# Kernel optimization log

Measured on AMD Instinct MI355X. Metric: run time of the kernel, lower is better.

The kernel has to match this reference:

```python
import jax, jax.numpy as jnp
import numpy as np
from jax.scipy.special import logsumexp

NTRANS = 40          # 2 * nbase * (nbase + 1) with nbase = 4
NBASE = 4
# cat-mod index groups: A:[can, 6mA_1, 6mA_2], C:[can, 5mC], G:[can], T:[can, modT]
CAN_INDICES = [np.array([0, 1, 2]), np.array([0, 3]), np.array([0]), np.array([0, 4])]


def global_norm_flipflop(scores):
    """scores: [T, N, 40] -> globally normalized scores [T, N, 40]."""
    T, N, C = scores.shape
    nbase = NBASE
    two_nb = 2 * nbase
    # fwd = zeros, then normalized: logZ0 = log(2*nbase)
    logZ0 = jnp.full((N, 1), jnp.log(float(two_nb)), scores.dtype)
    fwd0 = jnp.full((N, two_nb), -jnp.log(float(two_nb)), scores.dtype)

    def step(carry, scores_t):
        fwd, logZ = carry
        # [N, nbase+1, 2*nbase]
        curr = fwd[:, None, :] + scores_t.reshape(N, nbase + 1, two_nb)
        base1 = logsumexp(curr[:, :nbase, :], axis=2)                 # [N, nbase]
        base2 = jnp.logaddexp(curr[:, nbase, :nbase], curr[:, nbase, nbase:])  # [N, nbase]
        new_state = jnp.concatenate([base1, base2], axis=1)           # [N, 2*nbase]
        factors = logsumexp(new_state, axis=1, keepdims=True)         # [N, 1]
        new_state = new_state - factors
        return (new_state, logZ + factors), None

    (fwd, logZ), _ = jax.lax.scan(step, (fwd0, logZ0), scores)
    return scores - logZ[None, :, :] / T


def setup_inputs() -> dict:
    key = jax.random.key(0)
    k1, k2, k3 = jax.random.split(key, 3)
    T, N, D, S = 2000, 256, 256, 45
    x = jax.random.normal(k1, (T, N, D), dtype=jnp.float32)
    W = jax.random.normal(k2, (S, D), dtype=jnp.float32) * (1.0 / np.sqrt(D))
    b = jax.random.normal(k3, (S,), dtype=jnp.float32) * 0.5
    return {"x": x, "W": W, "b": b}


def reference(x, W, b):
    # Linear: [T, N, D] @ [D, S] + b
    y = jnp.einsum("tnd,sd->tns", x, W) + b
    trans_scores = 5.0 * jnp.tanh(y[:, :, :NTRANS])
    cat_mod_scores = y[:, :, NTRANS:]                 # [T, N, nmod+1] = [T, N, 5]
    norm_trans = global_norm_flipflop(trans_scores)   # [T, N, 40]
    mod_layers = [jax.nn.log_softmax(cat_mod_scores[:, :, idx], axis=2)
                  for idx in CAN_INDICES]
    cat_mods = jnp.concatenate(mod_layers, axis=2)    # [T, N, 8]
    return jnp.concatenate([norm_trans, cat_mods], axis=2)  # [T, N, 48]
```

## Files before the change

### kernel.cpp

```cpp
#include <hip/hip_runtime.h>
#include <hip/hip_bf16.h>
#include <math.h>

#define TT 2000
#define NN 256
#define DD 256
#define SS 45
#define SOUT 48
#define NTRANS_C 40
#define CHUNKS 40
#define CLEN 50
#define BK 32
#define NCH (DD / BK)
#define XPAD 40

typedef __attribute__((ext_vector_type(8))) short bf16x8;
typedef __attribute__((ext_vector_type(4))) float f32x4;

__device__ inline ushort f2bf_rne(float f) {
    unsigned u = __float_as_uint(f);
    unsigned r = u + 0x7fffu + ((u >> 16) & 1u);
    return (ushort)(r >> 16);
}
__device__ __forceinline__ int cvtpk(float lo, float hi) {
    int r;
    asm("v_cvt_pk_bf16_f32 %0, %1, %2" : "=v"(r) : "v"(lo), "v"(hi));
    return r;
}
__device__ __forceinline__ float bf2f(ushort h) {
    return __uint_as_float(((unsigned)h) << 16);
}
__device__ __host__ __forceinline__ constexpr int sidx(int c) {
    return (c < 32) ? (4 * (c & 7) + (c >> 3))
         : (c < 36) ? (32 + 2 * (c - 32))
         : (c < 40) ? (32 + 2 * (c - 36) + 1)
         : c;
}
__device__ __forceinline__ int swz_idx(int s, int koff) {
    return s * DD + ((((koff >> 3) ^ (s & 7)) << 3) | (koff & 7));
}

__global__ __launch_bounds__(256) void kPrep(const float* __restrict__ W,
                                             const float* __restrict__ b,
                                             ushort* __restrict__ Whi,
                                             float* __restrict__ b48) {
    const int s = blockIdx.x;
    const int k = threadIdx.x;
    const float wv = (s < SS) ? W[s * DD + k] : 0.f;
    Whi[s * DD + k] = f2bf_rne(wv);
    if (k == 0) b48[s] = (s < SS) ? b[s] : 0.f;
}

__global__ __launch_bounds__(512, 6) void kA_mfma(const float* __restrict__ x,
                                                  const ushort* __restrict__ Whi,
                                                  const float* __restrict__ b48,
                                                  ushort* __restrict__ sc) {
    __shared__ ushort Wl[SOUT * DD];
    __shared__ ushort xw[8][16 * XPAD];
    const int tid = threadIdx.x;
    for (int idx = tid; idx < SOUT * (DD / 8); idx += 512) {
        const int s = idx >> 5;
        const int c8 = (idx & 31) * 8;
        const uint4 v = *reinterpret_cast<const uint4*>(Whi + s * DD + c8);
        *reinterpret_cast<uint4*>(&Wl[swz_idx(s, c8)]) = v;
    }
    __syncthreads();

    const int l = tid & 63, w = tid >> 6;
    const long m0 = (long)blockIdx.x * 128;
    const int r16 = l & 15;
    const int kg = l >> 4;
    const int lrow = l >> 3;
    const int lcol = (l & 7) * 4;
    const float* xp = x + (m0 + w * 16 + lrow) * DD + lcol;
    const float* xq = xp + 8 * DD;
    ushort* xs = xw[w];
    int2* xw0 = reinterpret_cast<int2*>(&xs[lrow * XPAD + lcol]);
    int2* xw1 = reinterpret_cast<int2*>(&xs[(lrow + 8) * XPAD + lcol]);
    const bf16x8* xrd = reinterpret_cast<const bf16x8*>(&xs[r16 * XPAD + kg * 8]);

    f32x4 acc[3] = {{0, 0, 0, 0}, {0, 0, 0, 0}, {0, 0, 0, 0}};

    float4 pf[2][2];
    pf[0][0] = *reinterpret_cast<const float4*>(xp + 0);
    pf[0][1] = *reinterpret_cast<const float4*>(xq + 0);
    pf[1][0] = *reinterpret_cast<const float4*>(xp + BK);
    pf[1][1] = *reinterpret_cast<const float4*>(xq + BK);

#pragma unroll
    for (int c = 0; c < NCH; ++c) {
        const float4 pa = pf[c & 1][0];
        const float4 qa = pf[c & 1][1];
        xw0->x = cvtpk(pa.x, pa.y);
        xw0->y = cvtpk(pa.z, pa.w);
        xw1->x = cvtpk(qa.x, qa.y);
        xw1->y = cvtpk(qa.z, qa.w);
        if (c + 2 < NCH) {
            pf[c & 1][0] = *reinterpret_cast<const float4*>(xp + (c + 2) * BK);
            pf[c & 1][1] = *reinterpret_cast<const float4*>(xq + (c + 2) * BK);
        }
        __builtin_amdgcn_sched_barrier(0);
        const bf16x8 a = *xrd;
        const int koff = c * BK + kg * 8;
        const bf16x8 b0 = *reinterpret_cast<const bf16x8*>(&Wl[swz_idx(0 * 16 + r16, koff)]);
        const bf16x8 b1 = *reinterpret_cast<const bf16x8*>(&Wl[swz_idx(1 * 16 + r16, koff)]);
        const bf16x8 b2 = *reinterpret_cast<const bf16x8*>(&Wl[swz_idx(2 * 16 + r16, koff)]);
        acc[0] = __builtin_amdgcn_mfma_f32_16x16x32_bf16(a, b0, acc[0], 0, 0, 0);
        acc[1] = __builtin_amdgcn_mfma_f32_16x16x32_bf16(a, b1, acc[1], 0, 0, 0);
        acc[2] = __builtin_amdgcn_mfma_f32_16x16x32_bf16(a, b2, acc[2], 0, 0, 0);
    }

    __syncthreads();
    ushort* se = Wl;
#pragma unroll
    for (int jt = 0; jt < 3; ++jt) {
        const int col = jt * 16 + r16;
        const float bias = b48[col];
        int si;
        if (jt < 2) si = 4 * (col & 7) + (col >> 3);
        else if (r16 < 8) si = (r16 < 4) ? (32 + 2 * r16) : (32 + 2 * (r16 - 4) + 1);
        else si = 40 + (r16 - 8);
#pragma unroll
        for (int r = 0; r < 4; ++r) {
            const int lr = w * 16 + kg * 4 + r;
            const float y = acc[jt][r] + bias;
            float v;
            if (col < NTRANS_C) {
                const float e = __expf(2.f * y);
                v = 5.f * (1.f - 2.f / (e + 1.f));
            } else {
                v = y;
            }
            se[lr * SOUT + si] = f2bf_rne(v);
        }
    }
    __syncthreads();
    const uint4* su = reinterpret_cast<const uint4*>(se);
    uint4* du = reinterpret_cast<uint4*>(sc + m0 * SOUT);
    du[tid] = su[tid];
    if (tid < 256) du[512 + tid] = su[512 + tid];
}

#define DPP_XOR1 0xB1
#define DPP_XOR2 0x4E

__device__ inline float fmax_x1(float v) {
    const int d = __builtin_amdgcn_mov_dpp(__float_as_int(v), DPP_XOR1, 0xF, 0xF, true);
    return fmaxf(v, __int_as_float(d));
}
__device__ inline float fmax_x2(float v) {
    const int d = __builtin_amdgcn_mov_dpp(__float_as_int(v), DPP_XOR2, 0xF, 0xF, true);
    return fmaxf(v, __int_as_float(d));
}
__device__ inline float add_x1(float v) {
    const int d = __builtin_amdgcn_mov_dpp(__float_as_int(v), DPP_XOR1, 0xF, 0xF, true);
    return v + __int_as_float(d);
}
__device__ inline float add_x2(float v) {
    const int d = __builtin_amdgcn_mov_dpp(__float_as_int(v), DPP_XOR2, 0xF, 0xF, true);
    return v + __int_as_float(d);
}
__device__ inline float swz4(float v) {
    return __int_as_float(__builtin_amdgcn_ds_swizzle(__float_as_int(v), 0x101F));
}
__device__ inline float fmax_x4(float v) { return fmaxf(v, swz4(v)); }
__device__ inline float add_x4(float v) { return v + swz4(v); }
__device__ inline float sum8(float v) { return add_x4(add_x2(add_x1(v))); }
__device__ inline float max8(float v) { return fmax_x4(fmax_x2(fmax_x1(v))); }

__global__ __launch_bounds__(64) void kB_scan(const ushort* __restrict__ sc,
                                              float* __restrict__ gbuf) {
    __shared__ float elp[2][2][48][2];
    const int n = blockIdx.x;
    const int l = threadIdx.x;
    const int h = l >> 5;
    const int l32 = l & 31;
    const int d = l32 & 3;
    const int q = l32 >> 2;
    const int ch = blockIdx.y * 2 + h;
    const long stride = (long)NN * SOUT;
    const ushort* sp = sc + ((long)(ch * CLEN) * NN + n) * SOUT;

    float Plo = (d == q) ? 1.f : 0.f;
    float Phi = (4 + d == q) ? 1.f : 0.f;
    int scale = 0;

    {
        float2 e2 = { __expf(bf2f(sp[l32])), __expf(bf2f(sp[stride + l32])) };
        *reinterpret_cast<float2*>(&elp[h][0][l32][0]) = e2;
        if (l32 < 8) {
            float2 f2 = { __expf(bf2f(sp[32 + l32])),
                          __expf(bf2f(sp[stride + 32 + l32])) };
            *reinterpret_cast<float2*>(&elp[h][0][32 + l32][0]) = f2;
        }
    }

    for (int u = 0; u < CLEN / 2; ++u) {
        const float* eb = &elp[h][u & 1][0][0];
        if (u + 1 < CLEN / 2) {
            const ushort* r2 = sp + (long)(2 * u + 2) * stride;
            const ushort* r3 = sp + (long)(2 * u + 3) * stride;
            float2 e2 = { __expf(bf2f(r2[l32])), __expf(bf2f(r3[l32])) };
            *reinterpret_cast<float2*>(&elp[h][(u + 1) & 1][l32][0]) = e2;
            if (l32 < 8) {
                float2 f2 = { __expf(bf2f(r2[32 + l32])),
                              __expf(bf2f(r3[32 + l32])) };
                *reinterpret_cast<float2*>(&elp[h][(u + 1) & 1][32 + l32][0]) = f2;
            }
        }
        const float4 rA = *reinterpret_cast<const float4*>(eb + (4 * d) * 2);
        const float4 rB = *reinterpret_cast<const float4*>(eb + (4 * d + 2) * 2);
        const float4 rC = *reinterpret_cast<const float4*>(eb + (16 + 4 * d) * 2);
        const float4 rD = *reinterpret_cast<const float4*>(eb + (16 + 4 * d + 2) * 2);
        const float4 rE = *reinterpret_cast<const float4*>(eb + (32 + 2 * d) * 2);

        {
            float v0 = fmaf(Plo, rA.x, Phi * rC.x);
            float v1 = fmaf(Plo, rA.z, Phi * rC.z);
            float v2 = fmaf(Plo, rB.x, Phi * rD.x);
            float v3 = fmaf(Plo, rB.z, Phi * rD.z);
            v0 = add_x2(add_x1(v0));
            v1 = add_x2(add_x1(v1));
            v2 = add_x2(add_x1(v2));
            v3 = add_x2(add_x1(v3));
            const float PhiN = fmaf(Plo, rE.x, Phi * rE.z);
            const float pa_ = (d & 1) ? v1 : v0;
            const float pb_ = (d & 1) ? v3 : v2;
            Plo = (d & 2) ? pb_ : pa_;
            Phi = PhiN;
        }
        {
            float v0 = fmaf(Plo, rA.y, Phi * rC.y);
            float v1 = fmaf(Plo, rA.w, Phi * rC.w);
            float v2 = fmaf(Plo, rB.y, Phi * rD.y);
            float v3 = fmaf(Plo, rB.w, Phi * rD.w);
            v0 = add_x2(add_x1(v0));
            v1 = add_x2(add_x1(v1));
            v2 = add_x2(add_x1(v2));
            v3 = add_x2(add_x1(v3));
            const float PhiN = fmaf(Plo, rE.y, Phi * rE.w);
            const float pa_ = (d & 1) ? v1 : v0;
            const float pb_ = (d & 1) ? v3 : v2;
            Plo = (d & 2) ? pb_ : pa_;
            Phi = PhiN;
        }
        if (u & 1) {
            const float Mx = fmax_x2(fmax_x1(fmaxf(Plo, Phi)));
            const int ex = ((__float_as_int(Mx) >> 23) & 255) - 127;
            const float s = __int_as_float((unsigned)(127 - ex) << 23);
            Plo *= s;
            Phi *= s;
            scale += ex;
        }
    }
    const float base = (float)scale * 0.6931471805599453f;
    float* gb = gbuf + ((long)(n * CHUNKS + ch)) * 64;
    gb[q * 8 + d] = __logf(Plo) + base;
    gb[q * 8 + 4 + d] = __logf(Phi) + base;
}

__device__ inline float lse8(float v) {
    const float m = max8(v);
    return m + __logf(sum8(__expf(v - m)));
}
__device__ inline float lse64(float v) {
    float m = v;
#pragma unroll
    for (int d = 1; d < 64; d <<= 1) m = fmaxf(m, __shfl_xor(m, d));
    float e = __expf(v - m);
#pragma unroll
    for (int d = 1; d < 64; d <<= 1) e += __shfl_xor(e, d);
    return m + __logf(e);
}

__global__ __launch_bounds__(64) void kC_combine(const float* __restrict__ gbuf,
                                                 float* __restrict__ logZT) {
    const int n = blockIdx.x;
    const int l = threadIdx.x;
    const int gi = (l & 7) * 8 + (l >> 3);
    float g[CHUNKS];
#pragma unroll
    for (int c = 0; c < CHUNKS; ++c)
        g[c] = gbuf[((long)(n * CHUNKS + c)) * 64 + gi];
    float u = -logf(8.f);
#pragma unroll
    for (int c = 0; c < CHUNKS; ++c) {
        const float nu = lse8(g[c] + u);
        u = __shfl(nu, ((l & 7) << 3) | (l >> 3));
    }
    const float z = lse64(u);
    if (l == 0) logZT[n] = z / (float)TT;
}

__global__ __launch_bounds__(128) void kD_final(const ushort* __restrict__ sc,
                                                const float* __restrict__ logZT,
                                                float* __restrict__ out) {
    __shared__ float dout[128 * SOUT];
    const int tid = threadIdx.x;
    const long row0 = (long)blockIdx.x * 128;
    const long row = row0 + tid;
    const int n = (int)(row & (NN - 1));
    const float z = logZT[n];
    const ushort* srow = sc + row * SOUT;
    float st[48];
#pragma unroll
    for (int i = 0; i < 6; ++i) {
        const uint4 qv = reinterpret_cast<const uint4*>(srow)[i];
        const unsigned wv[4] = {qv.x, qv.y, qv.z, qv.w};
#pragma unroll
        for (int t = 0; t < 4; ++t) {
            st[8 * i + 2 * t]     = __uint_as_float(wv[t] << 16);
            st[8 * i + 2 * t + 1] = __uint_as_float(wv[t] & 0xffff0000u);
        }
    }
    float* a = &dout[tid * SOUT];
#pragma unroll
    for (int c = 0; c < 40; ++c) a[c] = st[sidx(c)] - z;
    const float y40 = st[40], y41 = st[41], y42 = st[42], y43 = st[43], y44 = st[44];
    const float m3 = fmaxf(fmaxf(y40, y41), y42);
    const float l3 = m3 + __logf(__expf(y40 - m3) + __expf(y41 - m3) + __expf(y42 - m3));
    a[40] = y40 - l3; a[41] = y41 - l3; a[42] = y42 - l3;
    const float mA = fmaxf(y40, y43);
    const float lA = mA + __logf(__expf(y40 - mA) + __expf(y43 - mA));
    a[43] = y40 - lA; a[44] = y43 - lA;
    a[45] = 0.f;
    const float mB = fmaxf(y40, y44);
    const float lB = mB + __logf(__expf(y40 - mB) + __expf(y44 - mB));
    a[46] = y40 - lB; a[47] = y44 - lB;
    __syncthreads();
    const float4* sf = reinterpret_cast<const float4*>(dout);
    float4* df = reinterpret_cast<float4*>(out + row0 * SOUT);
#pragma unroll
    for (int kq = 0; kq < 12; ++kq)
        df[kq * 128 + tid] = sf[kq * 128 + tid];
}

extern "C" void kernel_launch(void* const* d_in, const int* in_sizes, int n_in,
                              void* d_out, int out_size, void* d_ws, size_t ws_size,
                              hipStream_t stream) {
    const float* x = (const float*)d_in[0];
    const float* W = (const float*)d_in[1];
    const float* b = (const float*)d_in[2];
    float* out = (float*)d_out;

    ushort* sc   = (ushort*)d_ws;
    float* gbuf  = (float*)((char*)d_ws + 49152000);
    float* logZT = gbuf + (long)NN * CHUNKS * 64;
    float* b48   = logZT + NN;
    ushort* Whi  = (ushort*)(b48 + SOUT);

    hipLaunchKernelGGL(kPrep, dim3(SOUT), dim3(DD), 0, stream, W, b, Whi, b48);
    hipLaunchKernelGGL(kA_mfma, dim3((TT * NN) / 128), dim3(512), 0, stream, x, Whi, b48, sc);
    hipLaunchKernelGGL(kB_scan, dim3(NN, CHUNKS / 2), dim3(64), 0, stream, sc, gbuf);
    hipLaunchKernelGGL(kC_combine, dim3(NN), dim3(64), 0, stream, gbuf, logZT);
    hipLaunchKernelGGL(kD_final, dim3((TT * NN) / 128), dim3(128), 0, stream, sc, logZT, out);
}
```

Baseline: 186.4 us.

## Prefetch scan inputs two steps ahead in registers and widen scan blocks

The chunked flip-flop scan kernel now issues global loads for timestep pairs two iterations ahead into a three-slot register ring. This hides global memory latency behind the serial recurrence instead of loading right before use. Blocks also grow from 64 to 256 threads, so each block handles 8 chunks instead of 2, giving fewer and larger workgroups. The cost is more registers per thread and a fully unrolled loop, which could lower occupancy.

```diff
diff --git a/kernel.cpp b/kernel.cpp
--- a/kernel.cpp
+++ b/kernel.cpp
@@ -168,16 +168,16 @@
 __device__ inline float sum8(float v) { return add_x4(add_x2(add_x1(v))); }
 __device__ inline float max8(float v) { return fmax_x4(fmax_x2(fmax_x1(v))); }
 
-__global__ __launch_bounds__(64) void kB_scan(const ushort* __restrict__ sc,
-                                              float* __restrict__ gbuf) {
-    __shared__ float elp[2][2][48][2];
+__global__ __launch_bounds__(256) void kB_scan(const ushort* __restrict__ sc,
+                                               float* __restrict__ gbuf) {
+    __shared__ float elp[8][2][48][2];
     const int n = blockIdx.x;
-    const int l = threadIdx.x;
-    const int h = l >> 5;
-    const int l32 = l & 31;
+    const int tid = threadIdx.x;
+    const int h = tid >> 5;
+    const int l32 = tid & 31;
     const int d = l32 & 3;
     const int q = l32 >> 2;
-    const int ch = blockIdx.y * 2 + h;
+    const int ch = blockIdx.y * 8 + h;
     const long stride = (long)NN * SOUT;
     const ushort* sp = sc + ((long)(ch * CLEN) * NN + n) * SOUT;
 
@@ -195,19 +195,34 @@
         }
     }
 
+    ushort qa[3], qb[3], qc[3], qd[3];
+#pragma unroll
+    for (int v = 0; v < 2; ++v) {
+        const ushort* rA_ = sp + (long)(2 * v + 2) * stride;
+        const ushort* rB_ = sp + (long)(2 * v + 3) * stride;
+        qa[v] = rA_[l32];
+        qb[v] = rB_[l32];
+        if (l32 < 8) { qc[v] = rA_[32 + l32]; qd[v] = rB_[32 + l32]; }
+    }
+
+#pragma unroll
     for (int u = 0; u < CLEN / 2; ++u) {
-        const float* eb = &elp[h][u & 1][0][0];
-        if (u + 1 < CLEN / 2) {
-            const ushort* r2 = sp + (long)(2 * u + 2) * stride;
-            const ushort* r3 = sp + (long)(2 * u + 3) * stride;
-            float2 e2 = { __expf(bf2f(r2[l32])), __expf(bf2f(r3[l32])) };
+        if (u <= CLEN / 2 - 2) {
+            float2 e2 = { __expf(bf2f(qa[u % 3])), __expf(bf2f(qb[u % 3])) };
             *reinterpret_cast<float2*>(&elp[h][(u + 1) & 1][l32][0]) = e2;
             if (l32 < 8) {
-                float2 f2 = { __expf(bf2f(r2[32 + l32])),
-                              __expf(bf2f(r3[32 + l32])) };
+                float2 f2 = { __expf(bf2f(qc[u % 3])), __expf(bf2f(qd[u % 3])) };
                 *reinterpret_cast<float2*>(&elp[h][(u + 1) & 1][32 + l32][0]) = f2;
             }
         }
+        if (u + 2 <= CLEN / 2 - 2) {
+            const ushort* rA_ = sp + (long)(2 * u + 6) * stride;
+            const ushort* rB_ = sp + (long)(2 * u + 7) * stride;
+            qa[(u + 2) % 3] = rA_[l32];
+            qb[(u + 2) % 3] = rB_[l32];
+            if (l32 < 8) { qc[(u + 2) % 3] = rA_[32 + l32]; qd[(u + 2) % 3] = rB_[32 + l32]; }
+        }
+        const float* eb = &elp[h][u & 1][0][0];
         const float4 rA = *reinterpret_cast<const float4*>(eb + (4 * d) * 2);
         const float4 rB = *reinterpret_cast<const float4*>(eb + (4 * d + 2) * 2);
         const float4 rC = *reinterpret_cast<const float4*>(eb + (16 + 4 * d) * 2);
@@ -351,7 +366,7 @@
 
     hipLaunchKernelGGL(kPrep, dim3(SOUT), dim3(DD), 0, stream, W, b, Whi, b48);
     hipLaunchKernelGGL(kA_mfma, dim3((TT * NN) / 128), dim3(512), 0, stream, x, Whi, b48, sc);
-    hipLaunchKernelGGL(kB_scan, dim3(NN, CHUNKS / 2), dim3(64), 0, stream, sc, gbuf);
+    hipLaunchKernelGGL(kB_scan, dim3(NN, CHUNKS / 8), dim3(256), 0, stream, sc, gbuf);
     hipLaunchKernelGGL(kC_combine, dim3(NN), dim3(64), 0, stream, gbuf, logZT);
     hipLaunchKernelGGL(kD_final, dim3((TT * NN) / 128), dim3(128), 0, stream, sc, logZT, out);
 }
```

Result: faster. 179.3 us (-3.8%).
